# Kernel optimization log

Measured on AMD Instinct MI355X. Metric: run time of the kernel, lower is better.

## Reference

```python
import jax, jax.numpy as jnp
import numpy as np

B, L, HID = 2, 2048, 2048
H, KVH, HD = 8, 1, 256
GROUPS = H // KVH
THETA = 10000.0
NEG_INF = -1e9


def _rope_cos_sin(seq_len, hd):
    inv_freq = 1.0 / (THETA ** (jnp.arange(0, hd, 2, dtype=jnp.float32) / hd))
    t = jnp.arange(seq_len, dtype=jnp.float32)
    freqs = jnp.outer(t, inv_freq)                # [L, hd/2]
    emb = jnp.concatenate([freqs, freqs], axis=-1)  # [L, hd]
    return jnp.cos(emb), jnp.sin(emb)


def _rotate_half(x):
    x1, x2 = jnp.split(x, 2, axis=-1)
    return jnp.concatenate([-x2, x1], axis=-1)


def _apply_rope(x, cos, sin):
    # x: [B, h, L, hd]; cos/sin: [L, hd] broadcast over batch/heads
    return x * cos[None, None] + _rotate_half(x) * sin[None, None]


def setup_inputs() -> dict:
    key = jax.random.key(0)
    kx, kq, kk, kv, ko = jax.random.split(key, 5)
    s = lambda fan_in: 1.0 / np.sqrt(fan_in)
    x = jax.random.normal(kx, (B, L, HID), dtype=jnp.float32)
    Wq = jax.random.normal(kq, (HID, H * HD), dtype=jnp.float32) * s(HID)
    Wk = jax.random.normal(kk, (HID, KVH * HD), dtype=jnp.float32) * s(HID)
    Wv = jax.random.normal(kv, (HID, KVH * HD), dtype=jnp.float32) * s(HID)
    Wo = jax.random.normal(ko, (H * HD, HID), dtype=jnp.float32) * s(H * HD)
    # causal additive mask, same semantics as SDPA attn_mask (float, additive)
    causal = jnp.tril(jnp.ones((L, L), dtype=bool))
    mask = jnp.where(causal, 0.0, NEG_INF).astype(jnp.float32)[None, None]
    return {"x": x, "Wq": Wq, "Wk": Wk, "Wv": Wv, "Wo": Wo, "mask": mask}


def reference(x, Wq, Wk, Wv, Wo, mask):
    # projections -> [B, h, L, hd]
    q = (x @ Wq).reshape(B, L, H, HD).transpose(0, 2, 1, 3)
    k = (x @ Wk).reshape(B, L, KVH, HD).transpose(0, 2, 1, 3)
    v = (x @ Wv).reshape(B, L, KVH, HD).transpose(0, 2, 1, 3)
    cos, sin = _rope_cos_sin(L, HD)
    q = _apply_rope(q, cos, sin)
    k = _apply_rope(k, cos, sin)
    # GQA: replicate kv heads (repeat_interleave over head dim)
    k = jnp.repeat(k, GROUPS, axis=1)
    v = jnp.repeat(v, GROUPS, axis=1)
    scale = HD ** -0.5
    scores = jnp.einsum("bhqd,bhkd->bhqk", q, k) * scale + mask
    attn = jax.nn.softmax(scores.astype(jnp.float32), axis=-1).astype(q.dtype)
    out = jnp.einsum("bhqk,bhkd->bhqd", attn, v)
    out = out.transpose(0, 2, 1, 3).reshape(B, L, H * HD)
    return out @ Wo
```

## Files before the change

kernel.cpp:

```cpp
#include <hip/hip_runtime.h>

typedef unsigned short u16;
typedef __attribute__((ext_vector_type(8))) short short8x;
typedef __attribute__((ext_vector_type(4))) float f32x4;

#define B_ 2
#define L_ 2048
#define HID_ 2048
#define H_ 8
#define HD_ 256

__device__ __forceinline__ u16 f2bf(float f) {
  union { float f; unsigned u; } v; v.f = f;
  unsigned r = v.u + 0x7FFFu + ((v.u >> 16) & 1u);
  return (u16)(r >> 16);
}
__device__ __forceinline__ float bf2f(u16 u) {
  union { unsigned u; float f; } v; v.u = ((unsigned)u) << 16;
  return v.f;
}

__device__ __forceinline__ void gload_lds16(const void* g, void* l) {
  __builtin_amdgcn_global_load_lds((const __attribute__((address_space(1))) unsigned*)g,
                                   (__attribute__((address_space(3))) unsigned*)l, 16, 0, 0);
}

__global__ __launch_bounds__(256) void cvt_x_kernel(const float4* __restrict__ in,
                                                    u16* __restrict__ out) {
  int idx = blockIdx.x * 256 + threadIdx.x;
  float4 v = in[idx];
  u16* o = out + (size_t)idx * 4;
  o[0] = f2bf(v.x); o[1] = f2bf(v.y); o[2] = f2bf(v.z); o[3] = f2bf(v.w);
}

__global__ __launch_bounds__(256) void cvt_wt_kernel(const float* __restrict__ W,
                                                     u16* __restrict__ Wt, int K, int N) {
  __shared__ float tile[32][33];
  int n0 = blockIdx.x * 32, k0 = blockIdx.y * 32;
  int tx = threadIdx.x, ty = threadIdx.y;
#pragma unroll
  for (int i = 0; i < 32; i += 8)
    tile[ty + i][tx] = W[(size_t)(k0 + ty + i) * N + n0 + tx];
  __syncthreads();
#pragma unroll
  for (int i = 0; i < 32; i += 8)
    Wt[(size_t)(n0 + ty + i) * K + k0 + tx] = f2bf(tile[tx][ty + i]);
}

__global__ __launch_bounds__(256) void rope_kernel(const u16* __restrict__ in,
                                                   u16* __restrict__ out, int nh_shift,
                                                   int in_stride, int in_off, float scale) {
  int idx = blockIdx.x * 256 + threadIdx.x;
  int nh = 1 << nh_shift;
  int d = idx & 127;
  int t = idx >> 7;
  int h = t & (nh - 1);
  int row = t >> nh_shift;
  int l = row & (L_ - 1);
  int b = row >> 11;
  size_t ibase = (size_t)row * in_stride + in_off + h * 256 + d;
  float x1 = bf2f(in[ibase]);
  float x2 = bf2f(in[ibase + 128]);
  float f = exp2f(-(float)d * (13.287712379549449f / 128.0f));
  float ang = (float)l * f;
  float s, c;
  sincosf(ang, &s, &c);
  size_t obase = ((size_t)(b * nh + h) * L_ + l) * 256 + d;
  out[obase] = f2bf((x1 * c - x2 * s) * scale);
  out[obase + 128] = f2bf((x2 * c + x1 * s) * scale);
}

__global__ __launch_bounds__(256) void vt_kernel(const u16* __restrict__ qkvproj,
                                                 u16* __restrict__ vt) {
  __shared__ u16 tile[32][33];
  int l0 = blockIdx.x * 32, d0 = blockIdx.y * 32, b = blockIdx.z;
  int tx = threadIdx.x, ty = threadIdx.y;
#pragma unroll
  for (int i = 0; i < 32; i += 8)
    tile[ty + i][tx] = qkvproj[((size_t)b * 2048 + l0 + ty + i) * 2560 + 2304 + d0 + tx];
  __syncthreads();
#pragma unroll
  for (int i = 0; i < 32; i += 8)
    vt[((size_t)b * 256 + d0 + ty + i) * 2048 + l0 + tx] = tile[tx][ty + i];
}

template <int F32OUT>
__global__ __launch_bounds__(512) void gemmtb_kernel(const u16* __restrict__ A,
                                                     const u16* __restrict__ Bt,
                                                     void* __restrict__ Cv,
                                                     int M, int N, int K) {
  __shared__ __attribute__((aligned(16))) u16 As[3][256 * 64];
  __shared__ __attribute__((aligned(16))) u16 Bs[3][128 * 64];
  const int tid = threadIdx.x, lane = tid & 63, w = tid >> 6;
  const int wr = w >> 1, wc = w & 1;
  const int l15 = lane & 15, l4 = lane >> 4;
  const int nbx = gridDim.x;
  int flat = blockIdx.y * nbx + blockIdx.x;
  int nwg = nbx * gridDim.y;
  int q8 = nwg >> 3, r8 = nwg & 7;
  int xcd = flat & 7, idx8 = flat >> 3;
  int neu = (xcd < r8 ? xcd * (q8 + 1) : r8 * (q8 + 1) + (xcd - r8) * q8) + idx8;
  const int m0 = (neu / nbx) * 256, n0 = (neu % nbx) * 128;
  const int NT = K >> 6;

  f32x4 acc[4][4] = {};
  short8x a[4][2], b[4][2];

#define STAGE_A(t, s)                                                           \
  {                                                                             \
    _Pragma("unroll") for (int i = 0; i < 4; ++i) {                             \
      int c = i * 512 + tid;                                                    \
      int row = c >> 3, j = (c & 7) ^ (row & 7);                                \
      gload_lds16(A + (size_t)(m0 + row) * K + (t) * 64 + j * 8,                \
                  (char*)&As[s][0] + (i * 512 + w * 64) * 16);                  \
    }                                                                           \
  }
#define STAGE_B(t, s)                                                           \
  {                                                                             \
    _Pragma("unroll") for (int i = 0; i < 2; ++i) {                             \
      int c = i * 512 + tid;                                                    \
      int row = c >> 3, j = (c & 7) ^ (row & 7);                                \
      gload_lds16(Bt + (size_t)(n0 + row) * K + (t) * 64 + j * 8,               \
                  (char*)&Bs[s][0] + (i * 512 + w * 64) * 16);                  \
    }                                                                           \
  }
#define RD_A(s, mi, ks)                                                         \
  (*(const short8x*)((const char*)&As[s][0] +                                   \
      ((((wr * 64 + (mi) * 16 + l15) * 128 + ((ks) * 4 + l4) * 16)) ^           \
       ((l15 & 7) << 4))))
#define RD_B(s, ni, ks)                                                         \
  (*(const short8x*)((const char*)&Bs[s][0] +                                   \
      ((((wc * 64 + (ni) * 16 + l15) * 128 + ((ks) * 4 + l4) * 16)) ^           \
       ((l15 & 7) << 4))))

  STAGE_A(0, 0);
  STAGE_B(0, 0);
  STAGE_A(1, 1);
  STAGE_B(1, 1);
  asm volatile("s_waitcnt vmcnt(6)" ::: "memory");
  __builtin_amdgcn_s_barrier();

  for (int t = 0; t < NT; ++t) {
    const int cur = t % 3, nxt = (t + 2) % 3;
    const bool ns = (t + 2 < NT);
#pragma unroll
    for (int mi = 0; mi < 4; ++mi) { a[mi][0] = RD_A(cur, mi, 0); a[mi][1] = RD_A(cur, mi, 1); }
#pragma unroll
    for (int ni = 0; ni < 2; ++ni) { b[ni][0] = RD_B(cur, ni, 0); b[ni][1] = RD_B(cur, ni, 1); }
    if (ns) STAGE_A(t + 2, nxt);
    __builtin_amdgcn_s_barrier();
    __builtin_amdgcn_s_setprio(1);
#pragma unroll
    for (int mi = 0; mi < 4; ++mi)
#pragma unroll
      for (int ni = 0; ni < 2; ++ni) {
        acc[mi][ni] = __builtin_amdgcn_mfma_f32_16x16x32_bf16(a[mi][0], b[ni][0], acc[mi][ni], 0, 0, 0);
        acc[mi][ni] = __builtin_amdgcn_mfma_f32_16x16x32_bf16(a[mi][1], b[ni][1], acc[mi][ni], 0, 0, 0);
      }
    __builtin_amdgcn_s_setprio(0);
    __builtin_amdgcn_s_barrier();
#pragma unroll
    for (int ni = 2; ni < 4; ++ni) { b[ni][0] = RD_B(cur, ni, 0); b[ni][1] = RD_B(cur, ni, 1); }
    if (ns) STAGE_B(t + 2, nxt);
    __builtin_amdgcn_s_barrier();
    __builtin_amdgcn_s_setprio(1);
#pragma unroll
    for (int mi = 0; mi < 4; ++mi)
#pragma unroll
      for (int ni = 2; ni < 4; ++ni) {
        acc[mi][ni] = __builtin_amdgcn_mfma_f32_16x16x32_bf16(a[mi][0], b[ni][0], acc[mi][ni], 0, 0, 0);
        acc[mi][ni] = __builtin_amdgcn_mfma_f32_16x16x32_bf16(a[mi][1], b[ni][1], acc[mi][ni], 0, 0, 0);
      }
    __builtin_amdgcn_s_setprio(0);
    if (ns) asm volatile("s_waitcnt vmcnt(6)" ::: "memory");
    else    asm volatile("s_waitcnt vmcnt(0)" ::: "memory");
    __builtin_amdgcn_s_barrier();
  }
#pragma unroll
  for (int mi = 0; mi < 4; ++mi) {
#pragma unroll
    for (int ni = 0; ni < 4; ++ni) {
      int gcol = n0 + wc * 64 + ni * 16 + l15;
#pragma unroll
      for (int r = 0; r < 4; ++r) {
        int grow = m0 + wr * 64 + mi * 16 + l4 * 4 + r;
        if (F32OUT)
          ((float*)Cv)[(size_t)grow * N + gcol] = acc[mi][ni][r];
        else
          ((u16*)Cv)[(size_t)grow * N + gcol] = f2bf(acc[mi][ni][r]);
      }
    }
  }
#undef STAGE_A
#undef STAGE_B
#undef RD_A
#undef RD_B
}

__global__ __launch_bounds__(512) void flash_kernel(const u16* __restrict__ qkv,
                                                    const u16* __restrict__ kb,
                                                    const u16* __restrict__ vt,
                                                    u16* __restrict__ attn_o) {
  __shared__ __attribute__((aligned(16))) u16 Kbuf[2][64 * 256];
  __shared__ __attribute__((aligned(16))) u16 Vbuf[2][256 * 64];
  __shared__ __attribute__((aligned(16))) u16 Ps[8 * 16 * 64];
  const int x = blockIdx.x;
  const int p = x >> 4;
  const int bh = x & 15;
  const int b = bh >> 3;
  const int h = bh & 7;
  const int tid = threadIdx.x, lane = tid & 63, w = tid >> 6;
  const int l15 = lane & 15, l4 = lane >> 4;
  const int j = (w < 4) ? (31 - p) : p;
  const int q0 = j * 64 + (w & 3) * 16;
  const int nt = (31 - p) + 1;

  const int lpos = q0 + l15;
  const u16* qrow = qkv + ((size_t)(b * 2048 + lpos) * 2560 + h * 256);
  short8x qf[8];
#pragma unroll
  for (int kc = 0; kc < 8; ++kc)
    qf[kc] = *(const short8x*)(qrow + kc * 32 + l4 * 8);
#pragma unroll
  for (int kc = 0; kc < 4; ++kc) {
    short8x lo = qf[kc], hi = qf[kc + 4];
#pragma unroll
    for (int jj = 0; jj < 8; ++jj) {
      int d = kc * 32 + l4 * 8 + jj;
      float f = exp2f(-(float)d * (13.287712379549449f / 128.0f));
      float ang = (float)lpos * f;
      float s, c;
      sincosf(ang, &s, &c);
      float x1 = bf2f((u16)lo[jj]), x2 = bf2f((u16)hi[jj]);
      lo[jj] = (short)f2bf((x1 * c - x2 * s) * 0.0625f);
      hi[jj] = (short)f2bf((x2 * c + x1 * s) * 0.0625f);
    }
    qf[kc] = lo;
    qf[kc + 4] = hi;
  }

  f32x4 o[16] = {};
  float mrow = -3e38f, srow = 0.f;

  const u16* kbase = kb + (size_t)b * (L_ * 256);
  const u16* vbase = vt + (size_t)b * (256 * L_);

#define STAGE(t, s)                                                            \
  {                                                                            \
    _Pragma("unroll") for (int i2 = 0; i2 < 4; ++i2) {                         \
      int c = i2 * 512 + tid;                                                  \
      int rk = c >> 5, cck = c & 31, jk = cck ^ (rk & 7);                      \
      gload_lds16(kbase + (size_t)((t) * 64 + rk) * 256 + jk * 8,              \
                  (char*)&Kbuf[s][0] + (i2 * 512 + w * 64) * 16);              \
      int rd = c >> 3, ccv = c & 7, jv = ccv ^ (rd & 7);                       \
      gload_lds16(vbase + (size_t)rd * L_ + (t) * 64 + jv * 8,                 \
                  (char*)&Vbuf[s][0] + (i2 * 512 + w * 64) * 16);              \
    }                                                                          \
  }

  STAGE(0, 0);
  asm volatile("s_waitcnt vmcnt(0)" ::: "memory");
  __syncthreads();

  for (int t = 0; t < nt; ++t) {
    if (t + 1 < nt) STAGE(t + 1, (t + 1) & 1);
    if (t <= j) {
      const char* Kb = (const char*)&Kbuf[t & 1][0];
      const char* Vb = (const char*)&Vbuf[t & 1][0];

      f32x4 sacc[4] = {};
      __builtin_amdgcn_s_setprio(1);
#pragma unroll
      for (int kc = 0; kc < 8; ++kc)
#pragma unroll
        for (int n = 0; n < 4; ++n) {
          int row = n * 16 + l15;
          short8x kf = *(const short8x*)(Kb +
              ((row * 512 + kc * 64 + l4 * 16) ^ ((row & 7) << 4)));
          sacc[n] = __builtin_amdgcn_mfma_f32_16x16x32_bf16(kf, qf[kc], sacc[n], 0, 0, 0);
        }
      __builtin_amdgcn_s_setprio(0);
      float pp[4][4];
      const bool dm = (t == j);
      const int qg = q0 + l15;
      float pm = -3e38f;
#pragma unroll
      for (int n = 0; n < 4; ++n)
#pragma unroll
        for (int r = 0; r < 4; ++r) {
          int kvg = t * 64 + n * 16 + l4 * 4 + r;
          float v = sacc[n][r];
          if (dm && (kvg > qg)) v = -1e30f;
          pp[n][r] = v;
          pm = fmaxf(pm, v);
        }
      pm = fmaxf(pm, __shfl_xor(pm, 16));
      pm = fmaxf(pm, __shfl_xor(pm, 32));
      const bool defer = __all(pm <= mrow + 8.f);
      float mn, alpha;
      if (defer) {
        mn = mrow;
      } else {
        mn = fmaxf(mrow, pm);
        alpha = __expf(mrow - mn);
        mrow = mn;
      }
      float rs = 0.f;
#pragma unroll
      for (int n = 0; n < 4; ++n)
#pragma unroll
        for (int r = 0; r < 4; ++r) {
          pp[n][r] = __expf(pp[n][r] - mn);
          rs += pp[n][r];
        }
      rs += __shfl_xor(rs, 16);
      rs += __shfl_xor(rs, 32);
      if (defer) {
        srow += rs;
      } else {
        srow = srow * alpha + rs;
        float av[4];
#pragma unroll
        for (int r = 0; r < 4; ++r)
          av[r] = __shfl(alpha, l4 * 4 + r, 16);
#pragma unroll
        for (int ff = 0; ff < 16; ++ff) {
          o[ff][0] *= av[0]; o[ff][1] *= av[1];
          o[ff][2] *= av[2]; o[ff][3] *= av[3];
        }
      }
#pragma unroll
      for (int n = 0; n < 4; ++n)
#pragma unroll
        for (int r = 0; r < 4; r += 2) {
          unsigned pk;
          asm("v_cvt_pk_bf16_f32 %0, %1, %2" : "=v"(pk) : "v"(pp[n][r]), "v"(pp[n][r + 1]));
          *(unsigned*)((char*)Ps + w * 2048 +
                       ((l15 * 128 + (n * 16 + l4 * 4 + r) * 2) ^ ((l15 & 7) << 4))) = pk;
        }
      asm volatile("s_waitcnt lgkmcnt(0)" ::: "memory");
      short8x paf[2];
#pragma unroll
      for (int kc2 = 0; kc2 < 2; ++kc2)
        paf[kc2] = *(const short8x*)((const char*)Ps + w * 2048 +
            ((l15 * 128 + kc2 * 64 + l4 * 16) ^ ((l15 & 7) << 4)));
      __builtin_amdgcn_s_setprio(1);
#pragma unroll
      for (int kc2 = 0; kc2 < 2; ++kc2)
#pragma unroll
        for (int ff = 0; ff < 16; ++ff) {
          int rd = ff * 16 + l15;
          short8x vf = *(const short8x*)(Vb +
              ((rd * 128 + kc2 * 64 + l4 * 16) ^ ((rd & 7) << 4)));
          o[ff] = __builtin_amdgcn_mfma_f32_16x16x32_bf16(paf[kc2], vf, o[ff], 0, 0, 0);
        }
      __builtin_amdgcn_s_setprio(0);
    }
    asm volatile("s_waitcnt vmcnt(0)" ::: "memory");
    __syncthreads();
  }
  float sv[4];
#pragma unroll
  for (int r = 0; r < 4; ++r)
    sv[r] = __shfl(srow, l4 * 4 + r, 16);
#pragma unroll
  for (int r = 0; r < 4; ++r) {
    float inv = 1.0f / sv[r];
    int grow = q0 + l4 * 4 + r;
    size_t base = ((size_t)b * L_ + grow) * (size_t)(H_ * HD_) + h * 256;
#pragma unroll
    for (int ff = 0; ff < 16; ++ff)
      attn_o[base + ff * 16 + l15] = f2bf(o[ff][r] * inv);
  }
#undef STAGE
}

extern "C" void kernel_launch(void* const* d_in, const int* in_sizes, int n_in,
                              void* d_out, int out_size, void* d_ws, size_t ws_size,
                              hipStream_t stream) {
  const float* x  = (const float*)d_in[0];
  const float* Wq = (const float*)d_in[1];
  const float* Wk = (const float*)d_in[2];
  const float* Wv = (const float*)d_in[3];
  const float* Wo = (const float*)d_in[4];
  float* out = (float*)d_out;
  char* ws = (char*)d_ws;
  size_t off = 0;
  auto alloc = [&](size_t bytes) {
    void* p = ws + off;
    off = (off + bytes + 255) & ~(size_t)255;
    return p;
  };
  u16* wqkv_t  = (u16*)alloc(2560ull * 2048 * 2);
  u16* wo_t    = (u16*)alloc(2048ull * 2048 * 2);
  u16* xbf     = (u16*)alloc(4096ull * 2048 * 2);
  u16* qkvproj = (u16*)alloc(4096ull * 2560 * 2);
  u16* kb      = (u16*)alloc(4096ull * 256 * 2);
  u16* vtb     = (u16*)alloc(4096ull * 256 * 2);
  u16* attn_o  = xbf;

  cvt_x_kernel<<<8192, 256, 0, stream>>>((const float4*)x, xbf);
  cvt_wt_kernel<<<dim3(64, 64), dim3(32, 8), 0, stream>>>(Wq, wqkv_t, 2048, 2048);
  cvt_wt_kernel<<<dim3(8, 64),  dim3(32, 8), 0, stream>>>(Wk, wqkv_t + 2048ull * 2048, 2048, 256);
  cvt_wt_kernel<<<dim3(8, 64),  dim3(32, 8), 0, stream>>>(Wv, wqkv_t + 2304ull * 2048, 2048, 256);
  cvt_wt_kernel<<<dim3(64, 64), dim3(32, 8), 0, stream>>>(Wo, wo_t, 2048, 2048);

  gemmtb_kernel<0><<<dim3(20, 16), 512, 0, stream>>>(xbf, wqkv_t, qkvproj, 4096, 2560, 2048);

  rope_kernel<<<2048, 256, 0, stream>>>(qkvproj, kb, 0, 2560, 2048, 1.0f);
  vt_kernel<<<dim3(64, 8, 2), dim3(32, 8), 0, stream>>>(qkvproj, vtb);

  flash_kernel<<<256, 512, 0, stream>>>(qkvproj, kb, vtb, attn_o);

  gemmtb_kernel<1><<<dim3(16, 16), 512, 0, stream>>>(attn_o, wo_t, out, 4096, 2048, 2048);
}
```

Before: 219.4 us.

## Software-pipeline flash QK^T one tile ahead and precompute RoPE cos/sin table

The flash attention loop now computes the QK^T MFMAs for tile t+1 while softmax and PV for tile t run. K and V staging are split so each half of a buffer is refilled as soon as it is consumed, with partial vmcnt waits in place of full drains. RoPE cos/sin values are precomputed once into a table that both the K rope kernel and the Q rope in flash read, replacing per-element sincos. This adds registers for the extra score accumulators, which may lower occupancy, and it relies on exact vmcnt counting, which is fragile.

```diff
diff --git a/kernel.cpp b/kernel.cpp
--- a/kernel.cpp
+++ b/kernel.cpp
@@ -33,6 +33,16 @@
   o[0] = f2bf(v.x); o[1] = f2bf(v.y); o[2] = f2bf(v.z); o[3] = f2bf(v.w);
 }
 
+__global__ __launch_bounds__(256) void rope_tab_kernel(float2* __restrict__ tab) {
+  int idx = blockIdx.x * 256 + threadIdx.x;
+  int d = idx & 127;
+  int l = idx >> 7;
+  float f = exp2f(-(float)d * (13.287712379549449f / 128.0f));
+  float s, c;
+  sincosf((float)l * f, &s, &c);
+  tab[idx] = make_float2(c, s);
+}
+
 __global__ __launch_bounds__(256) void cvt_wt_kernel(const float* __restrict__ W,
                                                      u16* __restrict__ Wt, int K, int N) {
   __shared__ float tile[32][33];
@@ -48,26 +58,21 @@
 }
 
 __global__ __launch_bounds__(256) void rope_kernel(const u16* __restrict__ in,
-                                                   u16* __restrict__ out, int nh_shift,
-                                                   int in_stride, int in_off, float scale) {
+                                                   u16* __restrict__ out,
+                                                   const float2* __restrict__ tab,
+                                                   int in_stride, int in_off) {
   int idx = blockIdx.x * 256 + threadIdx.x;
-  int nh = 1 << nh_shift;
   int d = idx & 127;
-  int t = idx >> 7;
-  int h = t & (nh - 1);
-  int row = t >> nh_shift;
+  int row = idx >> 7;
   int l = row & (L_ - 1);
   int b = row >> 11;
-  size_t ibase = (size_t)row * in_stride + in_off + h * 256 + d;
+  size_t ibase = (size_t)row * in_stride + in_off + d;
   float x1 = bf2f(in[ibase]);
   float x2 = bf2f(in[ibase + 128]);
-  float f = exp2f(-(float)d * (13.287712379549449f / 128.0f));
-  float ang = (float)l * f;
-  float s, c;
-  sincosf(ang, &s, &c);
-  size_t obase = ((size_t)(b * nh + h) * L_ + l) * 256 + d;
-  out[obase] = f2bf((x1 * c - x2 * s) * scale);
-  out[obase + 128] = f2bf((x2 * c + x1 * s) * scale);
+  float2 cs = tab[l * 128 + d];
+  size_t obase = ((size_t)b * L_ + l) * 256 + d;
+  out[obase] = f2bf(x1 * cs.x - x2 * cs.y);
+  out[obase + 128] = f2bf(x2 * cs.x + x1 * cs.y);
 }
 
 __global__ __launch_bounds__(256) void vt_kernel(const u16* __restrict__ qkvproj,
@@ -200,6 +205,7 @@
 __global__ __launch_bounds__(512) void flash_kernel(const u16* __restrict__ qkv,
                                                     const u16* __restrict__ kb,
                                                     const u16* __restrict__ vt,
+                                                    const float2* __restrict__ tab,
                                                     u16* __restrict__ attn_o) {
   __shared__ __attribute__((aligned(16))) u16 Kbuf[2][64 * 256];
   __shared__ __attribute__((aligned(16))) u16 Vbuf[2][256 * 64];
@@ -227,13 +233,10 @@
 #pragma unroll
     for (int jj = 0; jj < 8; ++jj) {
       int d = kc * 32 + l4 * 8 + jj;
-      float f = exp2f(-(float)d * (13.287712379549449f / 128.0f));
-      float ang = (float)lpos * f;
-      float s, c;
-      sincosf(ang, &s, &c);
+      float2 cs = tab[lpos * 128 + d];
       float x1 = bf2f((u16)lo[jj]), x2 = bf2f((u16)hi[jj]);
-      lo[jj] = (short)f2bf((x1 * c - x2 * s) * 0.0625f);
-      hi[jj] = (short)f2bf((x2 * c + x1 * s) * 0.0625f);
+      lo[jj] = (short)f2bf((x1 * cs.x - x2 * cs.y) * 0.0625f);
+      hi[jj] = (short)f2bf((x2 * cs.x + x1 * cs.y) * 0.0625f);
     }
     qf[kc] = lo;
     qf[kc + 4] = hi;
@@ -245,41 +248,52 @@
   const u16* kbase = kb + (size_t)b * (L_ * 256);
   const u16* vbase = vt + (size_t)b * (256 * L_);
 
-#define STAGE(t, s)                                                            \
+#define KSTAGE(t, s)                                                           \
   {                                                                            \
     _Pragma("unroll") for (int i2 = 0; i2 < 4; ++i2) {                         \
       int c = i2 * 512 + tid;                                                  \
       int rk = c >> 5, cck = c & 31, jk = cck ^ (rk & 7);                      \
       gload_lds16(kbase + (size_t)((t) * 64 + rk) * 256 + jk * 8,              \
                   (char*)&Kbuf[s][0] + (i2 * 512 + w * 64) * 16);              \
+    }                                                                          \
+  }
+#define VSTAGE(t, s)                                                           \
+  {                                                                            \
+    _Pragma("unroll") for (int i2 = 0; i2 < 4; ++i2) {                         \
+      int c = i2 * 512 + tid;                                                  \
       int rd = c >> 3, ccv = c & 7, jv = ccv ^ (rd & 7);                       \
       gload_lds16(vbase + (size_t)rd * L_ + (t) * 64 + jv * 8,                 \
                   (char*)&Vbuf[s][0] + (i2 * 512 + w * 64) * 16);              \
     }                                                                          \
   }
-
-  STAGE(0, 0);
-  asm volatile("s_waitcnt vmcnt(0)" ::: "memory");
+#define QK_MFMA(s, dst)                                                        \
+  {                                                                            \
+    _Pragma("unroll") for (int kc = 0; kc < 8; ++kc)                           \
+        _Pragma("unroll") for (int n = 0; n < 4; ++n) {                        \
+      int row = n * 16 + l15;                                                  \
+      short8x kf = *(const short8x*)((const char*)&Kbuf[s][0] +                \
+          ((row * 512 + kc * 64 + l4 * 16) ^ ((row & 7) << 4)));               \
+      dst[n] = __builtin_amdgcn_mfma_f32_16x16x32_bf16(kf, qf[kc], dst[n], 0, 0, 0); \
+    }                                                                          \
+  }
+
+  KSTAGE(0, 0);
+  VSTAGE(0, 0);
+  if (nt > 1) { KSTAGE(1, 1); VSTAGE(1, 1); }
+  if (nt > 1) asm volatile("s_waitcnt vmcnt(8)" ::: "memory");
+  else        asm volatile("s_waitcnt vmcnt(0)" ::: "memory");
   __syncthreads();
+  f32x4 scur[4] = {};
+  QK_MFMA(0, scur);
 
   for (int t = 0; t < nt; ++t) {
-    if (t + 1 < nt) STAGE(t + 1, (t + 1) & 1);
+    if (t + 2 < nt) asm volatile("s_waitcnt vmcnt(4)" ::: "memory");
+    else            asm volatile("s_waitcnt vmcnt(0)" ::: "memory");
+    __builtin_amdgcn_s_barrier();
+    f32x4 snew[4] = {};
+    if (t + 1 < nt && t + 1 <= j) QK_MFMA((t + 1) & 1, snew);
+    if (t + 2 < nt) KSTAGE(t + 2, t & 1);
     if (t <= j) {
-      const char* Kb = (const char*)&Kbuf[t & 1][0];
-      const char* Vb = (const char*)&Vbuf[t & 1][0];
-
-      f32x4 sacc[4] = {};
-      __builtin_amdgcn_s_setprio(1);
-#pragma unroll
-      for (int kc = 0; kc < 8; ++kc)
-#pragma unroll
-        for (int n = 0; n < 4; ++n) {
-          int row = n * 16 + l15;
-          short8x kf = *(const short8x*)(Kb +
-              ((row * 512 + kc * 64 + l4 * 16) ^ ((row & 7) << 4)));
-          sacc[n] = __builtin_amdgcn_mfma_f32_16x16x32_bf16(kf, qf[kc], sacc[n], 0, 0, 0);
-        }
-      __builtin_amdgcn_s_setprio(0);
       float pp[4][4];
       const bool dm = (t == j);
       const int qg = q0 + l15;
@@ -289,7 +303,7 @@
 #pragma unroll
         for (int r = 0; r < 4; ++r) {
           int kvg = t * 64 + n * 16 + l4 * 4 + r;
-          float v = sacc[n][r];
+          float v = scur[n][r];
           if (dm && (kvg > qg)) v = -1e30f;
           pp[n][r] = v;
           pm = fmaxf(pm, v);
@@ -350,14 +364,16 @@
 #pragma unroll
         for (int ff = 0; ff < 16; ++ff) {
           int rd = ff * 16 + l15;
-          short8x vf = *(const short8x*)(Vb +
+          short8x vf = *(const short8x*)((const char*)&Vbuf[t & 1][0] +
               ((rd * 128 + kc2 * 64 + l4 * 16) ^ ((rd & 7) << 4)));
           o[ff] = __builtin_amdgcn_mfma_f32_16x16x32_bf16(paf[kc2], vf, o[ff], 0, 0, 0);
         }
       __builtin_amdgcn_s_setprio(0);
     }
-    asm volatile("s_waitcnt vmcnt(0)" ::: "memory");
-    __syncthreads();
+    __builtin_amdgcn_s_barrier();
+    if (t + 2 < nt) VSTAGE(t + 2, t & 1);
+#pragma unroll
+    for (int n = 0; n < 4; ++n) scur[n] = snew[n];
   }
   float sv[4];
 #pragma unroll
@@ -372,7 +388,9 @@
     for (int ff = 0; ff < 16; ++ff)
       attn_o[base + ff * 16 + l15] = f2bf(o[ff][r] * inv);
   }
-#undef STAGE
+#undef KSTAGE
+#undef VSTAGE
+#undef QK_MFMA
 }
 
 extern "C" void kernel_launch(void* const* d_in, const int* in_sizes, int n_in,
@@ -397,9 +415,11 @@
   u16* qkvproj = (u16*)alloc(4096ull * 2560 * 2);
   u16* kb      = (u16*)alloc(4096ull * 256 * 2);
   u16* vtb     = (u16*)alloc(4096ull * 256 * 2);
+  float2* rtab = (float2*)alloc(2048ull * 128 * 8);
   u16* attn_o  = xbf;
 
   cvt_x_kernel<<<8192, 256, 0, stream>>>((const float4*)x, xbf);
+  rope_tab_kernel<<<1024, 256, 0, stream>>>(rtab);
   cvt_wt_kernel<<<dim3(64, 64), dim3(32, 8), 0, stream>>>(Wq, wqkv_t, 2048, 2048);
   cvt_wt_kernel<<<dim3(8, 64),  dim3(32, 8), 0, stream>>>(Wk, wqkv_t + 2048ull * 2048, 2048, 256);
   cvt_wt_kernel<<<dim3(8, 64),  dim3(32, 8), 0, stream>>>(Wv, wqkv_t + 2304ull * 2048, 2048, 256);
@@ -407,10 +427,10 @@
 
   gemmtb_kernel<0><<<dim3(20, 16), 512, 0, stream>>>(xbf, wqkv_t, qkvproj, 4096, 2560, 2048);
 
-  rope_kernel<<<2048, 256, 0, stream>>>(qkvproj, kb, 0, 2560, 2048, 1.0f);
+  rope_kernel<<<2048, 256, 0, stream>>>(qkvproj + 2048, kb, rtab, 2560, 0);
   vt_kernel<<<dim3(64, 8, 2), dim3(32, 8), 0, stream>>>(qkvproj, vtb);
 
-  flash_kernel<<<256, 512, 0, stream>>>(qkvproj, kb, vtb, attn_o);
+  flash_kernel<<<256, 512, 0, stream>>>(qkvproj, kb, vtb, rtab, attn_o);
 
   gemmtb_kernel<1><<<dim3(16, 16), 512, 0, stream>>>(attn_o, wo_t, out, 4096, 2048, 2048);
 }
```

Measured after the change: 232.6 us. 1.06x slower.
